# Kernel tuning notes

Measured on AMD Instinct MI355X. Metric: run time of the kernel, lower is better.

## Reference

```python
import jax, jax.numpy as jnp
import numpy as np

HIDDEN = 128
E = 400000
NUM_GRAPHS = 512


def setup_inputs() -> dict:
    key = jax.random.key(0)
    ks = jax.random.split(key, 9)
    src = jax.random.normal(ks[0], (E, HIDDEN), dtype=jnp.float32)
    dst = jax.random.normal(ks[1], (E, HIDDEN), dtype=jnp.float32)
    edge_attr = jax.random.normal(ks[2], (E, HIDDEN), dtype=jnp.float32)
    u = jax.random.normal(ks[3], (NUM_GRAPHS, HIDDEN), dtype=jnp.float32)
    batch = jnp.sort(jax.random.randint(ks[4], (E,), 0, NUM_GRAPHS, dtype=jnp.int64))
    # MLP params: Linear(4*hidden -> hidden), ReLU, Linear(hidden -> hidden)
    in_dim = 4 * HIDDEN
    lim1 = 1.0 / np.sqrt(in_dim)
    lim2 = 1.0 / np.sqrt(HIDDEN)
    W1 = jax.random.uniform(ks[5], (in_dim, HIDDEN), minval=-lim1, maxval=lim1, dtype=jnp.float32)
    b1 = jax.random.uniform(ks[6], (HIDDEN,), minval=-lim1, maxval=lim1, dtype=jnp.float32)
    W2 = jax.random.uniform(ks[7], (HIDDEN, HIDDEN), minval=-lim2, maxval=lim2, dtype=jnp.float32)
    b2 = jax.random.uniform(ks[8], (HIDDEN,), minval=-lim2, maxval=lim2, dtype=jnp.float32)
    return {"src": src, "dst": dst, "edge_attr": edge_attr, "u": u,
            "batch": batch, "W1": W1, "b1": b1, "W2": W2, "b2": b2}


def reference(src, dst, edge_attr, u, batch, W1, b1, W2, b2):
    # gather global feature per edge, concat, 2-layer MLP
    x = jnp.concatenate([src, dst, edge_attr, u[batch]], axis=-1)  # [E, 4*hidden]
    h = jax.nn.relu(x @ W1 + b1)  # [E, hidden]
    return h @ W2 + b2            # [E, hidden]
```

## Files before the change

### kernel.cpp

```cpp
#include <hip/hip_runtime.h>

#define HID 128

typedef __attribute__((ext_vector_type(4)))  float f32x4;
typedef __attribute__((ext_vector_type(16))) float f32x16;
typedef __attribute__((ext_vector_type(8)))  short short8;
typedef __attribute__((ext_vector_type(4)))  short short4v;

static __device__ __forceinline__ unsigned cvt_pk_bf16(float lo, float hi) {
  unsigned r;
  asm("v_cvt_pk_bf16_f32 %0, %1, %2" : "=v"(r) : "v"(lo), "v"(hi));
  return r;
}

__global__ void prep_uc(const float* __restrict__ u, const float* __restrict__ W1,
                        const float* __restrict__ b1, float* __restrict__ Uc) {
  __shared__ float us[HID];
  const int g = blockIdx.x, n = threadIdx.x;
  us[n] = u[g * HID + n];
  __syncthreads();
  float acc = b1[n];
  const float* w = W1 + 3 * HID * HID + n;
  #pragma unroll 8
  for (int k = 0; k < HID; ++k) acc += us[k] * w[k * HID];
  Uc[g * HID + n] = acc;
}

__global__ __launch_bounds__(256, 2) void edge_mlp(
    const float* __restrict__ src, const float* __restrict__ dst,
    const float* __restrict__ ea, const int* __restrict__ batch,
    const float* __restrict__ W1, const float* __restrict__ W2,
    const float* __restrict__ b2, const float* __restrict__ Uc,
    float* __restrict__ out, int E, int nTiles) {
  __shared__ __align__(16) short Abuf[2][48 * 32 * 8];
  __shared__ __align__(16) short hbuf[16 * 32 * 8];

  const int tid  = threadIdx.x;
  const int lane = tid & 63;
  const int wave = tid >> 6;
  const int l31  = lane & 31;
  const int kh   = lane >> 5;
  const int ncol = wave * 32 + l31;
  const int cst  = (tid & 31) * 4;
  const int rb   = tid >> 5;

  if (blockIdx.x >= nTiles) return;

  f32x4 stg[12];
  #define STAGE_ISSUE(e0)                                                      \
    _Pragma("unroll")                                                          \
    for (int i = 0; i < 12; ++i) {                                             \
      const int a  = (i * 256 + tid) >> 10;                                    \
      const int r  = (i * 8 + rb) & 31;                                        \
      const int rg = min((e0) + r, E - 1);                                     \
      const float* gp = (a == 0 ? src : (a == 1 ? dst : ea));                  \
      stg[i] = *(const f32x4*)(gp + (long)rg * HID + cst);                     \
    }

  #define STAGE_WRITE(pb)                                                      \
    _Pragma("unroll")                                                          \
    for (int i = 0; i < 12; ++i) {                                             \
      const int a   = (i * 256 + tid) >> 10;                                   \
      const int r   = (i * 8 + rb) & 31;                                       \
      const int c16 = a * 16 + (cst >> 3);                                     \
      const int off = c16 * 256 + ((r ^ (c16 & 7)) << 3) + (cst & 4);          \
      union { unsigned u[2]; short4v s; } wpk;                                 \
      wpk.u[0] = cvt_pk_bf16(stg[i][0], stg[i][1]);                           \
      wpk.u[1] = cvt_pk_bf16(stg[i][2], stg[i][3]);                           \
      *(short4v*)&Abuf[pb][off] = wpk.s;                                       \
    }

  int t = blockIdx.x;
  const int G = gridDim.x;
  int p = 0;

  STAGE_ISSUE(t * 32)

  short8 B1f[24];
  #pragma unroll
  for (int s = 0; s < 24; ++s) {
    const float* pw = W1 + (long)(s * 16 + kh * 8) * HID + ncol;
    union { unsigned u[4]; short8 s8; } r;
    #pragma unroll
    for (int j = 0; j < 4; ++j)
      r.u[j] = cvt_pk_bf16(pw[(long)(2 * j) * HID], pw[(long)(2 * j + 1) * HID]);
    B1f[s] = r.s8;
  }
  short8 B2f[8];
  #pragma unroll
  for (int s = 0; s < 8; ++s) {
    const float* pw = W2 + (long)(s * 16 + kh * 8) * HID + ncol;
    union { unsigned u[4]; short8 s8; } r;
    #pragma unroll
    for (int j = 0; j < 4; ++j)
      r.u[j] = cvt_pk_bf16(pw[(long)(2 * j) * HID], pw[(long)(2 * j + 1) * HID]);
    B2f[s] = r.s8;
  }
  const float b2v = b2[ncol];

  STAGE_WRITE(0)
  asm volatile("s_waitcnt lgkmcnt(0)" ::: "memory");
  __builtin_amdgcn_s_barrier();

  while (true) {
    const int e0 = t * 32;
    const int tn = t + G;
    const bool more = (tn < nTiles);
    if (more) STAGE_ISSUE(tn * 32)

    f32x16 acc;
    #pragma unroll
    for (int i = 0; i < 16; ++i) acc[i] = 0.f;
    #pragma unroll
    for (int s = 0; s < 24; ++s) {
      const int c16 = 2 * s + kh;
      const short8 af = *(const short8*)&Abuf[p][c16 * 256 + ((l31 ^ (c16 & 7)) << 3)];
      acc = __builtin_amdgcn_mfma_f32_32x32x16_bf16(af, B1f[s], acc, 0, 0, 0);
    }

    const int gA = batch[e0];
    const int gB = batch[min(e0 + 31, E - 1)];
    if (gA == gB) {
      const float ucv = Uc[(long)gA * HID + ncol];
      #pragma unroll
      for (int i = 0; i < 16; ++i) acc[i] += ucv;
    } else {
      #pragma unroll
      for (int i = 0; i < 16; ++i) {
        const int crow = (i & 3) + 8 * (i >> 2) + 4 * kh;
        acc[i] += Uc[(long)batch[min(e0 + crow, E - 1)] * HID + ncol];
      }
    }

    const int hc = ncol >> 3;
    const int hs = ncol & 7;
    #pragma unroll
    for (int j = 0; j < 8; ++j) {
      const int i0 = 2 * j;
      const int r0 = (i0 & 3) + 8 * (i0 >> 2) + 4 * kh;
      const unsigned pk = cvt_pk_bf16(fmaxf(acc[i0], 0.f), fmaxf(acc[i0 + 1], 0.f));
      hbuf[hc * 256 + ((r0 ^ (hc & 7)) << 3) + hs]       = (short)(pk & 0xffffu);
      hbuf[hc * 256 + (((r0 + 1) ^ (hc & 7)) << 3) + hs] = (short)(pk >> 16);
    }

    asm volatile("s_waitcnt lgkmcnt(0)" ::: "memory");
    __builtin_amdgcn_s_barrier();

    f32x16 o;
    #pragma unroll
    for (int i = 0; i < 16; ++i) o[i] = 0.f;
    #pragma unroll
    for (int s = 0; s < 8; ++s) {
      const int c16 = 2 * s + kh;
      const short8 hf = *(const short8*)&hbuf[c16 * 256 + ((l31 ^ (c16 & 7)) << 3)];
      o = __builtin_amdgcn_mfma_f32_32x32x16_bf16(hf, B2f[s], o, 0, 0, 0);
    }

    #pragma unroll
    for (int i = 0; i < 16; ++i) {
      const int crow = (i & 3) + 8 * (i >> 2) + 4 * kh;
      const int e = e0 + crow;
      if (e < E) out[(long)e * HID + ncol] = o[i] + b2v;
    }

    if (!more) break;
    STAGE_WRITE(p ^ 1)
    asm volatile("s_waitcnt lgkmcnt(0)" ::: "memory");
    __builtin_amdgcn_s_barrier();
    p ^= 1;
    t = tn;
  }
  #undef STAGE_ISSUE
  #undef STAGE_WRITE
}

extern "C" void kernel_launch(void* const* d_in, const int* in_sizes, int n_in,
                              void* d_out, int out_size, void* d_ws, size_t ws_size,
                              hipStream_t stream) {
  const float* src   = (const float*)d_in[0];
  const float* dst   = (const float*)d_in[1];
  const float* ea    = (const float*)d_in[2];
  const float* u     = (const float*)d_in[3];
  const int*   batch = (const int*)d_in[4];
  const float* W1    = (const float*)d_in[5];
  const float* b1    = (const float*)d_in[6];
  const float* W2    = (const float*)d_in[7];
  const float* b2    = (const float*)d_in[8];
  float* out = (float*)d_out;
  float* Uc  = (float*)d_ws;

  const int E = in_sizes[0] / HID;
  const int G = in_sizes[3] / HID;

  prep_uc<<<G, HID, 0, stream>>>(u, W1, b1, Uc);

  const int nTiles = (E + 31) / 32;
  const int grid = nTiles < 512 ? nTiles : 512;
  edge_mlp<<<grid, 256, 0, stream>>>(src, dst, ea, batch, W1, W2, b2, Uc, out, E, nTiles);
}
```

Before: 621.2 us.

## Deepen prefetch pipeline and double-buffer hidden tile to drop a barrier per iteration

The loop now writes the next tile's staged registers into the alternate A buffer at the start of each iteration and, in the same pass, issues global loads for the tile after that, so prefetch runs two tiles ahead. The hidden-activation buffer is double-buffered, which lets the end-of-loop barrier be removed, leaving one barrier per tile. The batch/Uc lookup is hoisted before the first MFMA chain. This aims to hide global load latency and cut synchronisation, but it risks LDS races: the barrier that used to guard Abuf reuse is gone, and register pressure rises.

```diff
diff --git a/kernel.cpp b/kernel.cpp
--- a/kernel.cpp
+++ b/kernel.cpp
@@ -32,8 +32,8 @@
     const float* __restrict__ W1, const float* __restrict__ W2,
     const float* __restrict__ b2, const float* __restrict__ Uc,
     float* __restrict__ out, int E, int nTiles) {
-  __shared__ __align__(16) short Abuf[2][48 * 32 * 8];
-  __shared__ __align__(16) short hbuf[16 * 32 * 8];
+  __shared__ __align__(16) short Abuf[2][48 * 256];
+  __shared__ __align__(16) short hbuf[2][16 * 256];
 
   const int tid  = threadIdx.x;
   const int lane = tid & 63;
@@ -57,7 +57,7 @@
       stg[i] = *(const f32x4*)(gp + (long)rg * HID + cst);                     \
     }
 
-  #define STAGE_WRITE(pb)                                                      \
+  #define STAGE_WRITE_ISSUE(pb, e0n, di)                                       \
     _Pragma("unroll")                                                          \
     for (int i = 0; i < 12; ++i) {                                             \
       const int a   = (i * 256 + tid) >> 10;                                   \
@@ -65,14 +65,20 @@
       const int c16 = a * 16 + (cst >> 3);                                     \
       const int off = c16 * 256 + ((r ^ (c16 & 7)) << 3) + (cst & 4);          \
       union { unsigned u[2]; short4v s; } wpk;                                 \
-      wpk.u[0] = cvt_pk_bf16(stg[i][0], stg[i][1]);                           \
-      wpk.u[1] = cvt_pk_bf16(stg[i][2], stg[i][3]);                           \
+      wpk.u[0] = cvt_pk_bf16(stg[i][0], stg[i][1]);                            \
+      wpk.u[1] = cvt_pk_bf16(stg[i][2], stg[i][3]);                            \
       *(short4v*)&Abuf[pb][off] = wpk.s;                                       \
+      if (di) {                                                                \
+        const int rg = min((e0n) + r, E - 1);                                  \
+        const float* gp = (a == 0 ? src : (a == 1 ? dst : ea));                \
+        stg[i] = *(const f32x4*)(gp + (long)rg * HID + cst);                   \
+      }                                                                        \
     }
 
   int t = blockIdx.x;
   const int G = gridDim.x;
-  int p = 0;
+  int tn = t + G;
+  bool more = (tn < nTiles);
 
   STAGE_ISSUE(t * 32)
 
@@ -98,15 +104,21 @@
   }
   const float b2v = b2[ncol];
 
-  STAGE_WRITE(0)
+  STAGE_WRITE_ISSUE(0, tn * 32, more)
   asm volatile("s_waitcnt lgkmcnt(0)" ::: "memory");
   __builtin_amdgcn_s_barrier();
 
+  int p = 0, q = 0;
   while (true) {
-    const int e0 = t * 32;
-    const int tn = t + G;
-    const bool more = (tn < nTiles);
-    if (more) STAGE_ISSUE(tn * 32)
+    const int e0  = t * 32;
+    const int tnn = tn + G;
+
+    const int gA = batch[e0];
+    const int gB = batch[min(e0 + 31, E - 1)];
+    const bool uni = (gA == gB);
+    const float ucv = uni ? Uc[(long)gA * HID + ncol] : 0.f;
+
+    if (more) { STAGE_WRITE_ISSUE(p ^ 1, tnn * 32, (tnn < nTiles)) }
 
     f32x16 acc;
     #pragma unroll
@@ -118,10 +130,7 @@
       acc = __builtin_amdgcn_mfma_f32_32x32x16_bf16(af, B1f[s], acc, 0, 0, 0);
     }
 
-    const int gA = batch[e0];
-    const int gB = batch[min(e0 + 31, E - 1)];
-    if (gA == gB) {
-      const float ucv = Uc[(long)gA * HID + ncol];
+    if (uni) {
       #pragma unroll
       for (int i = 0; i < 16; ++i) acc[i] += ucv;
     } else {
@@ -139,8 +148,8 @@
       const int i0 = 2 * j;
       const int r0 = (i0 & 3) + 8 * (i0 >> 2) + 4 * kh;
       const unsigned pk = cvt_pk_bf16(fmaxf(acc[i0], 0.f), fmaxf(acc[i0 + 1], 0.f));
-      hbuf[hc * 256 + ((r0 ^ (hc & 7)) << 3) + hs]       = (short)(pk & 0xffffu);
-      hbuf[hc * 256 + (((r0 + 1) ^ (hc & 7)) << 3) + hs] = (short)(pk >> 16);
+      hbuf[q][hc * 256 + ((r0 ^ (hc & 7)) << 3) + hs]       = (short)(pk & 0xffffu);
+      hbuf[q][hc * 256 + (((r0 + 1) ^ (hc & 7)) << 3) + hs] = (short)(pk >> 16);
     }
 
     asm volatile("s_waitcnt lgkmcnt(0)" ::: "memory");
@@ -152,7 +161,7 @@
     #pragma unroll
     for (int s = 0; s < 8; ++s) {
       const int c16 = 2 * s + kh;
-      const short8 hf = *(const short8*)&hbuf[c16 * 256 + ((l31 ^ (c16 & 7)) << 3)];
+      const short8 hf = *(const short8*)&hbuf[q][c16 * 256 + ((l31 ^ (c16 & 7)) << 3)];
       o = __builtin_amdgcn_mfma_f32_32x32x16_bf16(hf, B2f[s], o, 0, 0, 0);
     }
 
@@ -164,14 +173,12 @@
     }
 
     if (!more) break;
-    STAGE_WRITE(p ^ 1)
-    asm volatile("s_waitcnt lgkmcnt(0)" ::: "memory");
-    __builtin_amdgcn_s_barrier();
-    p ^= 1;
-    t = tn;
+    p ^= 1; q ^= 1;
+    t = tn; tn = tnn;
+    more = (tn < nTiles);
   }
   #undef STAGE_ISSUE
-  #undef STAGE_WRITE
+  #undef STAGE_WRITE_ISSUE
 }
 
 extern "C" void kernel_launch(void* const* d_in, const int* in_sizes, int n_in,
```

New measurement: 738.1 us. +18.8%, slower.
